# Optimization experiments

Measured on AMD Instinct MI355X. Metric: run time of the kernel, lower is better.

Reference implementation:

```python
import jax, jax.numpy as jnp
import numpy as np

L, N, E, H = 1024, 8, 512, 8  # tgt/src len, batch, embed_dim, num_heads


def setup_inputs() -> dict:
    key = jax.random.key(0)
    ks = jax.random.split(key, 5)
    query = jax.random.normal(ks[0], (L, N, E), dtype=jnp.float32)
    # binary same-agent mask over (tgt, src) positions
    agent_aware_mask = (jax.random.uniform(ks[1], (L, L)) > 0.5).astype(jnp.float32)
    bound = 1.0 / np.sqrt(E)
    # agent-aware dot_product self-attn packs q,k,v,q_same,k_same -> (5E, E)
    in_proj_weight = jax.random.uniform(ks[2], (5 * E, E), jnp.float32, -bound, bound)
    in_proj_bias = jnp.zeros((5 * E,), jnp.float32)
    out_proj_weight = jax.random.uniform(ks[3], (E, E), jnp.float32, -bound, bound)
    out_proj_bias = jnp.zeros((E,), jnp.float32)
    return dict(query=query, in_proj_weight=in_proj_weight, in_proj_bias=in_proj_bias,
                out_proj_weight=out_proj_weight, out_proj_bias=out_proj_bias,
                agent_aware_mask=agent_aware_mask)


def _to_heads(x, tgt_len, bsz, num_heads, head_dim):
    # (L, N, E) -> (N*H, L, head_dim), matching torch's view+transpose
    return x.reshape(tgt_len, bsz * num_heads, head_dim).transpose(1, 0, 2)


def reference(query, in_proj_weight, in_proj_bias, out_proj_weight, out_proj_bias, agent_aware_mask):
    tgt_len, bsz, embed_dim = query.shape
    num_heads = H
    head_dim = embed_dim // num_heads
    scaling = float(head_dim) ** -0.5
    temperature = 1.0

    # packed input projection, chunked into 5: q, k, v, q_same, k_same
    proj = query @ in_proj_weight.T + in_proj_bias
    q, k, v, q_same, k_same = jnp.split(proj, 5, axis=-1)
    q = q * scaling
    q_same = q_same * scaling

    qh = _to_heads(q, tgt_len, bsz, num_heads, head_dim)
    kh = _to_heads(k, tgt_len, bsz, num_heads, head_dim)
    vh = _to_heads(v, tgt_len, bsz, num_heads, head_dim)
    qsh = _to_heads(q_same, tgt_len, bsz, num_heads, head_dim)
    ksh = _to_heads(k_same, tgt_len, bsz, num_heads, head_dim)

    attn_diff = jnp.einsum('bld,bsd->bls', qh, kh)    # cross-agent scores
    attn_same = jnp.einsum('bld,bsd->bls', qsh, ksh)  # same-agent scores

    mask = agent_aware_mask[None, :, :]  # broadcast over (N*H)
    logits = (attn_diff * (1.0 - mask) + attn_same * mask) / temperature

    attn_weights = jax.nn.softmax(logits, axis=-1)
    out = jnp.einsum('bls,bsd->bld', attn_weights, vh)  # (N*H, L, hd)
    out = out.transpose(1, 0, 2).reshape(tgt_len, bsz, embed_dim)
    return out @ out_proj_weight.T + out_proj_bias
```

## Files before the change

kernel.cpp:

```cpp
#include <hip/hip_runtime.h>


typedef float f32x4 __attribute__((ext_vector_type(4)));
typedef short s16x8 __attribute__((ext_vector_type(8)));
typedef unsigned short u16;
typedef u16 u16x4 __attribute__((ext_vector_type(4)));
typedef unsigned int u32x2 __attribute__((ext_vector_type(2)));

#define MFMA16(a, b, c) __builtin_amdgcn_mfma_f32_16x16x32_bf16((a), (b), (c), 0, 0, 0)

__device__ __forceinline__ u16 f2bf(float f) {
  __bf16 h = (__bf16)f;
  return __builtin_bit_cast(u16, h);
}
__device__ __forceinline__ unsigned int pack2(float a, float b) {
  return (unsigned int)f2bf(a) | ((unsigned int)f2bf(b) << 16);
}
__device__ __forceinline__ void gload_lds16(const u16* g, u16* l) {
  __builtin_amdgcn_global_load_lds(
      (const __attribute__((address_space(1))) void*)g,
      (__attribute__((address_space(3))) void*)l, 16, 0, 0);
}

__global__ __launch_bounds__(256) void cvt_swz(const float* __restrict__ in,
                                               u16* __restrict__ out, int n4) {
  int i = blockIdx.x * 256 + threadIdx.x;
  if (i >= n4) return;
  f32x4 v = *(const f32x4*)(in + (size_t)i * 4);
  int e = i << 2;
  int r = e >> 9;
  int k = e & 511;
  int ks = k ^ (((r >> 1) & 3) << 3);
  u16x4 o;
  o[0] = f2bf(v[0]); o[1] = f2bf(v[1]); o[2] = f2bf(v[2]); o[3] = f2bf(v[3]);
  *(u16x4*)(out + ((size_t)r << 9) + ks) = o;
}

__global__ __launch_bounds__(256) void gemm_inproj(
    const u16* __restrict__ X, const u16* __restrict__ W,
    const float* __restrict__ bias,
    u16* __restrict__ Qg, u16* __restrict__ Kg, u16* __restrict__ Vtg,
    u16* __restrict__ Qsg, u16* __restrict__ Ksg) {
  __shared__ __attribute__((aligned(16))) u16 At[128 * 32];
  __shared__ __attribute__((aligned(16))) u16 Bt[128 * 32];
  const int tid = threadIdx.x;
  const int lane = tid & 63, w = tid >> 6;
  const int lr = lane & 15, lq = lane >> 4;
  const int wr = w >> 1, wc = w & 1;
  const int tm = blockIdx.x * 128, tn = blockIdx.y * 128;

  f32x4 acc[4][4] = {};

  for (int k0 = 0; k0 < 512; k0 += 32) {
    if (k0) __syncthreads();
#pragma unroll
    for (int j = 0; j < 2; ++j) {
      const int c = (w * 2 + j) * 64 + lane;
      const int row = c >> 2;
      const int col = (c & 3) * 8;
      gload_lds16(X + (size_t)(tm + row) * 512 + k0 + col, At + (w * 2 + j) * 512);
      gload_lds16(W + (size_t)(tn + row) * 512 + k0 + col, Bt + (w * 2 + j) * 512);
    }
    __syncthreads();
    s16x8 af[4], bf[4];
#pragma unroll
    for (int mi = 0; mi < 4; ++mi) {
      const int row = wr * 64 + mi * 16 + lr;
      const int col = (lq * 8) ^ ((((tm + row) >> 1) & 3) << 3);
      af[mi] = *(const s16x8*)(At + row * 32 + col);
    }
#pragma unroll
    for (int ni = 0; ni < 4; ++ni) {
      const int row = wc * 64 + ni * 16 + lr;
      const int col = (lq * 8) ^ ((((tn + row) >> 1) & 3) << 3);
      bf[ni] = *(const s16x8*)(Bt + row * 32 + col);
    }
#pragma unroll
    for (int mi = 0; mi < 4; ++mi)
#pragma unroll
      for (int ni = 0; ni < 4; ++ni)
        acc[mi][ni] = MFMA16(af[mi], bf[ni], acc[mi][ni]);
  }

  const int chunk = tn >> 9;
  const float qscale = 0.125f * 1.4426950408889634f;
#pragma unroll
  for (int ni = 0; ni < 4; ++ni) {
    const int gc = tn + wc * 64 + ni * 16 + lr;
    const float bv = bias[gc];
    const int e = gc & 511;
    const int hh = e >> 6, dd = e & 63;
#pragma unroll
    for (int mi = 0; mi < 4; ++mi) {
#pragma unroll
      for (int r = 0; r < 4; ++r) {
        const int gr = tm + wr * 64 + mi * 16 + lq * 4 + r;
        const int l = gr >> 3, nn = gr & 7;
        const size_t base = (size_t)(nn * 8 + hh) << 16;
        float v = acc[mi][ni][r] + bv;
        if (chunk == 0) {
          Qg[base + l * 64 + dd] = f2bf(v * qscale);
        } else if (chunk == 3) {
          Qsg[base + l * 64 + dd] = f2bf(v * qscale);
        } else if (chunk == 1) {
          Kg[base + l * 64 + (dd ^ ((l & 7) << 3))] = f2bf(v);
        } else if (chunk == 4) {
          Ksg[base + l * 64 + (dd ^ ((l & 7) << 3))] = f2bf(v);
        } else {
          Vtg[base + (size_t)dd * 1024 + (l ^ ((dd & 7) << 3))] = f2bf(v);
        }
      }
    }
  }
}

__global__ __launch_bounds__(256) void attn_kernel(
    const u16* __restrict__ Qg, const u16* __restrict__ Kg,
    const u16* __restrict__ Vtg, const u16* __restrict__ Qsg,
    const u16* __restrict__ Ksg, const float* __restrict__ mask,
    u16* __restrict__ Og) {
  __shared__ __attribute__((aligned(16))) u16 Kt[64 * 64];
  __shared__ __attribute__((aligned(16))) u16 Kst[64 * 64];
  __shared__ __attribute__((aligned(16))) u16 Vt[64 * 64];
  __shared__ __attribute__((aligned(16))) u16 Pl[4][32 * 72];

  const int tid = threadIdx.x;
  const int lane = tid & 63, w = tid >> 6;
  const int lr = lane & 15, lq = lane >> 4;
  const int bh = blockIdx.y;
  const int q0 = blockIdx.x * 128;
  const size_t bbase = (size_t)bh << 16;
  const int nn = bh >> 3, hh = bh & 7;

  s16x8 qf[2][2], qsf[2][2];
#pragma unroll
  for (int nl = 0; nl < 2; ++nl) {
    const int l = q0 + w * 32 + nl * 16 + lr;
#pragma unroll
    for (int ks = 0; ks < 2; ++ks) {
      qf[nl][ks] = *(const s16x8*)(Qg + bbase + (size_t)l * 64 + ks * 32 + lq * 8);
      qsf[nl][ks] = *(const s16x8*)(Qsg + bbase + (size_t)l * 64 + ks * 32 + lq * 8);
    }
  }

  f32x4 oacc[4][2] = {};
  float m_run[2] = {-1e30f, -1e30f};
  float l_run[2] = {0.f, 0.f};

  for (int t = 0; t < 16; ++t) {
    const int s0 = t * 64;
    if (t) __syncthreads();
#pragma unroll
    for (int j = 0; j < 2; ++j) {
      const int cb = (w * 2 + j) * 64;
      const int c = cb + lane;
      const int row = c >> 3, col = (c & 7) * 8;
      gload_lds16(Kg + bbase + (size_t)(s0 + row) * 64 + col, Kt + cb * 8);
      gload_lds16(Ksg + bbase + (size_t)(s0 + row) * 64 + col, Kst + cb * 8);
      gload_lds16(Vtg + bbase + (size_t)row * 1024 + s0 + col, Vt + cb * 8);
    }
    __syncthreads();

    f32x4 sd[4][2] = {}, ss[4][2] = {};
#pragma unroll
    for (int smi = 0; smi < 4; ++smi) {
      const int srow = smi * 16 + lr;
#pragma unroll
      for (int ks = 0; ks < 2; ++ks) {
        const int off = srow * 64 + ((ks * 32 + lq * 8) ^ ((srow & 7) << 3));
        const s16x8 kf = *(const s16x8*)(Kt + off);
        const s16x8 ksf = *(const s16x8*)(Kst + off);
#pragma unroll
        for (int nl = 0; nl < 2; ++nl) {
          sd[smi][nl] = MFMA16(kf, qf[nl][ks], sd[smi][nl]);
          ss[smi][nl] = MFMA16(ksf, qsf[nl][ks], ss[smi][nl]);
        }
      }
    }

    float mt[2] = {-1e30f, -1e30f};
#pragma unroll
    for (int smi = 0; smi < 4; ++smi) {
#pragma unroll
      for (int nl = 0; nl < 2; ++nl) {
        const int l = q0 + w * 32 + nl * 16 + lr;
        const f32x4 mk =
            *(const f32x4*)(mask + (size_t)l * 1024 + s0 + smi * 16 + lq * 4);
#pragma unroll
        for (int r = 0; r < 4; ++r) {
          const float v = sd[smi][nl][r] + mk[r] * (ss[smi][nl][r] - sd[smi][nl][r]);
          sd[smi][nl][r] = v;
          mt[nl] = fmaxf(mt[nl], v);
        }
      }
    }
#pragma unroll
    for (int nl = 0; nl < 2; ++nl) {
      float m2 = fmaxf(mt[nl], __shfl_xor(mt[nl], 16));
      m2 = fmaxf(m2, __shfl_xor(m2, 32));
      mt[nl] = m2;
    }
    float mnew[2], scale[2];
#pragma unroll
    for (int nl = 0; nl < 2; ++nl) {
      mnew[nl] = fmaxf(m_run[nl], mt[nl]);
      scale[nl] = exp2f(m_run[nl] - mnew[nl]);
      m_run[nl] = mnew[nl];
    }
    float ts[2] = {0.f, 0.f};
#pragma unroll
    for (int smi = 0; smi < 4; ++smi)
#pragma unroll
      for (int nl = 0; nl < 2; ++nl)
#pragma unroll
        for (int r = 0; r < 4; ++r) {
          const float p = exp2f(sd[smi][nl][r] - mnew[nl]);
          sd[smi][nl][r] = p;
          ts[nl] += p;
        }
#pragma unroll
    for (int smi = 0; smi < 4; ++smi)
#pragma unroll
      for (int nl = 0; nl < 2; ++nl) {
        u32x2 pw;
        pw[0] = pack2(sd[smi][nl][0], sd[smi][nl][1]);
        pw[1] = pack2(sd[smi][nl][2], sd[smi][nl][3]);
        *(u32x2*)(&Pl[w][(nl * 16 + lr) * 72 + smi * 16 + lq * 4]) = pw;
      }
#pragma unroll
    for (int nl = 0; nl < 2; ++nl) {
      float s2 = ts[nl] + __shfl_xor(ts[nl], 16);
      s2 += __shfl_xor(s2, 32);
      l_run[nl] = l_run[nl] * scale[nl] + s2;
    }
#pragma unroll
    for (int dmi = 0; dmi < 4; ++dmi)
#pragma unroll
      for (int nl = 0; nl < 2; ++nl) oacc[dmi][nl] = oacc[dmi][nl] * scale[nl];

    asm volatile("s_waitcnt lgkmcnt(0)" ::: "memory");
    __builtin_amdgcn_sched_barrier(0);

#pragma unroll
    for (int ks = 0; ks < 2; ++ks) {
      s16x8 pf[2];
#pragma unroll
      for (int nl = 0; nl < 2; ++nl)
        pf[nl] = *(const s16x8*)(&Pl[w][(nl * 16 + lr) * 72 + ks * 32 + lq * 8]);
#pragma unroll
      for (int dmi = 0; dmi < 4; ++dmi) {
        const int d = dmi * 16 + lr;
        const s16x8 vf =
            *(const s16x8*)(Vt + d * 64 + ((ks * 32 + lq * 8) ^ ((d & 7) << 3)));
#pragma unroll
        for (int nl = 0; nl < 2; ++nl)
          oacc[dmi][nl] = MFMA16(vf, pf[nl], oacc[dmi][nl]);
      }
    }
  }

#pragma unroll
  for (int nl = 0; nl < 2; ++nl) {
    const float inv = 1.0f / l_run[nl];
    const int l = q0 + w * 32 + nl * 16 + lr;
    const int rout = l * 8 + nn;
#pragma unroll
    for (int dmi = 0; dmi < 4; ++dmi)
#pragma unroll
      for (int r = 0; r < 4; ++r) {
        const int d = dmi * 16 + lq * 4 + r;
        const int kout = hh * 64 + d;
        Og[(size_t)rout * 512 + (kout ^ (((rout >> 1) & 3) << 3))] =
            f2bf(oacc[dmi][nl][r] * inv);
      }
  }
}

__global__ __launch_bounds__(256) void gemm_outproj(
    const u16* __restrict__ A, const u16* __restrict__ W,
    const float* __restrict__ bias, float* __restrict__ out) {
  __shared__ __attribute__((aligned(16))) u16 At[128 * 32];
  __shared__ __attribute__((aligned(16))) u16 Bt[128 * 32];
  const int tid = threadIdx.x;
  const int lane = tid & 63, w = tid >> 6;
  const int lr = lane & 15, lq = lane >> 4;
  const int wr = w >> 1, wc = w & 1;
  const int tm = blockIdx.x * 128, tn = blockIdx.y * 128;

  f32x4 acc[4][4] = {};

  for (int k0 = 0; k0 < 512; k0 += 32) {
    if (k0) __syncthreads();
#pragma unroll
    for (int j = 0; j < 2; ++j) {
      const int c = (w * 2 + j) * 64 + lane;
      const int row = c >> 2;
      const int col = (c & 3) * 8;
      gload_lds16(A + (size_t)(tm + row) * 512 + k0 + col, At + (w * 2 + j) * 512);
      gload_lds16(W + (size_t)(tn + row) * 512 + k0 + col, Bt + (w * 2 + j) * 512);
    }
    __syncthreads();
    s16x8 af[4], bf[4];
#pragma unroll
    for (int mi = 0; mi < 4; ++mi) {
      const int row = wr * 64 + mi * 16 + lr;
      const int col = (lq * 8) ^ ((((tm + row) >> 1) & 3) << 3);
      af[mi] = *(const s16x8*)(At + row * 32 + col);
    }
#pragma unroll
    for (int ni = 0; ni < 4; ++ni) {
      const int row = wc * 64 + ni * 16 + lr;
      const int col = (lq * 8) ^ ((((tn + row) >> 1) & 3) << 3);
      bf[ni] = *(const s16x8*)(Bt + row * 32 + col);
    }
#pragma unroll
    for (int mi = 0; mi < 4; ++mi)
#pragma unroll
      for (int ni = 0; ni < 4; ++ni)
        acc[mi][ni] = MFMA16(af[mi], bf[ni], acc[mi][ni]);
  }

#pragma unroll
  for (int ni = 0; ni < 4; ++ni) {
    const int gc = tn + wc * 64 + ni * 16 + lr;
    const float bv = bias[gc];
#pragma unroll
    for (int mi = 0; mi < 4; ++mi)
#pragma unroll
      for (int r = 0; r < 4; ++r) {
        const int gr = tm + wr * 64 + mi * 16 + lq * 4 + r;
        out[(size_t)gr * 512 + gc] = acc[mi][ni][r] + bv;
      }
  }
}

extern "C" void kernel_launch(void* const* d_in, const int* in_sizes, int n_in,
                              void* d_out, int out_size, void* d_ws, size_t ws_size,
                              hipStream_t stream) {
  const float* query = (const float*)d_in[0];
  const float* w_in = (const float*)d_in[1];
  const float* b_in = (const float*)d_in[2];
  const float* w_out = (const float*)d_in[3];
  const float* b_out = (const float*)d_in[4];
  const float* mask = (const float*)d_in[5];

  char* ws = (char*)d_ws;
  u16* Xbf = (u16*)(ws + 0);
  u16* Wbf = (u16*)(ws + 8388608);
  u16* Wobf = (u16*)(ws + 11010048);
  u16* Qg = (u16*)(ws + 11534336);
  u16* Kg = (u16*)(ws + 19922944);
  u16* Vtg = (u16*)(ws + 28311552);
  u16* Qsg = (u16*)(ws + 36700160);
  u16* Ksg = (u16*)(ws + 45088768);
  u16* Og = (u16*)(ws + 53477376);

  hipLaunchKernelGGL(cvt_swz, dim3(4096), dim3(256), 0, stream, query, Xbf, 1048576);
  hipLaunchKernelGGL(cvt_swz, dim3(1280), dim3(256), 0, stream, w_in, Wbf, 327680);
  hipLaunchKernelGGL(cvt_swz, dim3(256), dim3(256), 0, stream, w_out, Wobf, 65536);
  hipLaunchKernelGGL(gemm_inproj, dim3(64, 20), dim3(256), 0, stream,
                     Xbf, Wbf, b_in, Qg, Kg, Vtg, Qsg, Ksg);
  hipLaunchKernelGGL(attn_kernel, dim3(8, 64), dim3(256), 0, stream,
                     Qg, Kg, Vtg, Qsg, Ksg, mask, Og);
  hipLaunchKernelGGL(gemm_outproj, dim3(64, 4), dim3(256), 0, stream,
                     Og, Wobf, b_out, (float*)d_out);
}
```

Before: 218.0 us.

## Bit-pack mask, shrink attention tile, lazy rescale, deeper K-step GEMMs

```diff
diff --git a/kernel.cpp b/kernel.cpp
--- a/kernel.cpp
+++ b/kernel.cpp
@@ -36,13 +36,20 @@
   *(u16x4*)(out + ((size_t)r << 9) + ks) = o;
 }
 
+__global__ __launch_bounds__(256) void mask_pack(const float* __restrict__ m,
+                                                 unsigned long long* __restrict__ out) {
+  int i = blockIdx.x * 256 + threadIdx.x;
+  unsigned long long b = __ballot(m[i] != 0.0f);
+  if ((threadIdx.x & 63) == 0) out[i >> 6] = b;
+}
+
 __global__ __launch_bounds__(256) void gemm_inproj(
     const u16* __restrict__ X, const u16* __restrict__ W,
     const float* __restrict__ bias,
     u16* __restrict__ Qg, u16* __restrict__ Kg, u16* __restrict__ Vtg,
     u16* __restrict__ Qsg, u16* __restrict__ Ksg) {
-  __shared__ __attribute__((aligned(16))) u16 At[128 * 32];
-  __shared__ __attribute__((aligned(16))) u16 Bt[128 * 32];
+  __shared__ __attribute__((aligned(16))) u16 At[128 * 64];
+  __shared__ __attribute__((aligned(16))) u16 Bt[128 * 64];
   const int tid = threadIdx.x;
   const int lane = tid & 63, w = tid >> 6;
   const int lr = lane & 15, lq = lane >> 4;
@@ -51,35 +58,38 @@
 
   f32x4 acc[4][4] = {};
 
-  for (int k0 = 0; k0 < 512; k0 += 32) {
+  for (int k0 = 0; k0 < 512; k0 += 64) {
     if (k0) __syncthreads();
 #pragma unroll
-    for (int j = 0; j < 2; ++j) {
-      const int c = (w * 2 + j) * 64 + lane;
-      const int row = c >> 2;
-      const int col = (c & 3) * 8;
-      gload_lds16(X + (size_t)(tm + row) * 512 + k0 + col, At + (w * 2 + j) * 512);
-      gload_lds16(W + (size_t)(tn + row) * 512 + k0 + col, Bt + (w * 2 + j) * 512);
+    for (int j = 0; j < 4; ++j) {
+      const int c = (w * 4 + j) * 64 + lane;
+      const int row = c >> 3;
+      const int col = (c & 7) * 8;
+      gload_lds16(X + (size_t)(tm + row) * 512 + k0 + col, At + (w * 4 + j) * 512);
+      gload_lds16(W + (size_t)(tn + row) * 512 + k0 + col, Bt + (w * 4 + j) * 512);
     }
     __syncthreads();
-    s16x8 af[4], bf[4];
-#pragma unroll
-    for (int mi = 0; mi < 4; ++mi) {
-      const int row = wr * 64 + mi * 16 + lr;
-      const int col = (lq * 8) ^ ((((tm + row) >> 1) & 3) << 3);
-      af[mi] = *(const s16x8*)(At + row * 32 + col);
-    }
-#pragma unroll
-    for (int ni = 0; ni < 4; ++ni) {
-      const int row = wc * 64 + ni * 16 + lr;
-      const int col = (lq * 8) ^ ((((tn + row) >> 1) & 3) << 3);
-      bf[ni] = *(const s16x8*)(Bt + row * 32 + col);
-    }
-#pragma unroll
-    for (int mi = 0; mi < 4; ++mi)
-#pragma unroll
-      for (int ni = 0; ni < 4; ++ni)
-        acc[mi][ni] = MFMA16(af[mi], bf[ni], acc[mi][ni]);
+#pragma unroll
+    for (int ks = 0; ks < 2; ++ks) {
+      s16x8 af[4], bf[4];
+#pragma unroll
+      for (int mi = 0; mi < 4; ++mi) {
+        const int row = wr * 64 + mi * 16 + lr;
+        const int col = ks * 32 + ((lq * 8) ^ ((((tm + row) >> 1) & 3) << 3));
+        af[mi] = *(const s16x8*)(At + row * 64 + col);
+      }
+#pragma unroll
+      for (int ni = 0; ni < 4; ++ni) {
+        const int row = wc * 64 + ni * 16 + lr;
+        const int col = ks * 32 + ((lq * 8) ^ ((((tn + row) >> 1) & 3) << 3));
+        bf[ni] = *(const s16x8*)(Bt + row * 64 + col);
+      }
+#pragma unroll
+      for (int mi = 0; mi < 4; ++mi)
+#pragma unroll
+        for (int ni = 0; ni < 4; ++ni)
+          acc[mi][ni] = MFMA16(af[mi], bf[ni], acc[mi][ni]);
+    }
   }
 
   const int chunk = tn >> 9;
@@ -114,38 +124,34 @@
   }
 }
 
-__global__ __launch_bounds__(256) void attn_kernel(
+__global__ __launch_bounds__(256, 4) void attn_kernel(
     const u16* __restrict__ Qg, const u16* __restrict__ Kg,
     const u16* __restrict__ Vtg, const u16* __restrict__ Qsg,
-    const u16* __restrict__ Ksg, const float* __restrict__ mask,
+    const u16* __restrict__ Ksg, const unsigned long long* __restrict__ Mp,
     u16* __restrict__ Og) {
   __shared__ __attribute__((aligned(16))) u16 Kt[64 * 64];
   __shared__ __attribute__((aligned(16))) u16 Kst[64 * 64];
   __shared__ __attribute__((aligned(16))) u16 Vt[64 * 64];
-  __shared__ __attribute__((aligned(16))) u16 Pl[4][32 * 72];
+  __shared__ __attribute__((aligned(16))) u16 Pl[4][16 * 72];
 
   const int tid = threadIdx.x;
   const int lane = tid & 63, w = tid >> 6;
   const int lr = lane & 15, lq = lane >> 4;
   const int bh = blockIdx.y;
-  const int q0 = blockIdx.x * 128;
+  const int q0 = blockIdx.x * 64;
   const size_t bbase = (size_t)bh << 16;
   const int nn = bh >> 3, hh = bh & 7;
-
-  s16x8 qf[2][2], qsf[2][2];
-#pragma unroll
-  for (int nl = 0; nl < 2; ++nl) {
-    const int l = q0 + w * 32 + nl * 16 + lr;
-#pragma unroll
-    for (int ks = 0; ks < 2; ++ks) {
-      qf[nl][ks] = *(const s16x8*)(Qg + bbase + (size_t)l * 64 + ks * 32 + lq * 8);
-      qsf[nl][ks] = *(const s16x8*)(Qsg + bbase + (size_t)l * 64 + ks * 32 + lq * 8);
-    }
-  }
-
-  f32x4 oacc[4][2] = {};
-  float m_run[2] = {-1e30f, -1e30f};
-  float l_run[2] = {0.f, 0.f};
+  const int l = q0 + w * 16 + lr;
+
+  s16x8 qf[2], qsf[2];
+#pragma unroll
+  for (int ks = 0; ks < 2; ++ks) {
+    qf[ks] = *(const s16x8*)(Qg + bbase + (size_t)l * 64 + ks * 32 + lq * 8);
+    qsf[ks] = *(const s16x8*)(Qsg + bbase + (size_t)l * 64 + ks * 32 + lq * 8);
+  }
+
+  f32x4 oacc[4] = {};
+  float m_run = -1e30f, l_run = 0.f;
 
   for (int t = 0; t < 16; ++t) {
     const int s0 = t * 64;
@@ -159,170 +165,156 @@
       gload_lds16(Ksg + bbase + (size_t)(s0 + row) * 64 + col, Kst + cb * 8);
       gload_lds16(Vtg + bbase + (size_t)row * 1024 + s0 + col, Vt + cb * 8);
     }
+    const unsigned long long mw = Mp[(size_t)l * 16 + t];
     __syncthreads();
 
-    f32x4 sd[4][2] = {}, ss[4][2] = {};
+    f32x4 sd[4] = {}, ss[4] = {};
+    __builtin_amdgcn_s_setprio(1);
 #pragma unroll
     for (int smi = 0; smi < 4; ++smi) {
       const int srow = smi * 16 + lr;
+      const int sw = (srow & 7) << 3;
 #pragma unroll
       for (int ks = 0; ks < 2; ++ks) {
-        const int off = srow * 64 + ((ks * 32 + lq * 8) ^ ((srow & 7) << 3));
+        const int off = srow * 64 + ((ks * 32 + lq * 8) ^ sw);
         const s16x8 kf = *(const s16x8*)(Kt + off);
-        const s16x8 ksf = *(const s16x8*)(Kst + off);
-#pragma unroll
-        for (int nl = 0; nl < 2; ++nl) {
-          sd[smi][nl] = MFMA16(kf, qf[nl][ks], sd[smi][nl]);
-          ss[smi][nl] = MFMA16(ksf, qsf[nl][ks], ss[smi][nl]);
-        }
-      }
-    }
-
-    float mt[2] = {-1e30f, -1e30f};
+        const s16x8 kfs = *(const s16x8*)(Kst + off);
+        sd[smi] = MFMA16(kf, qf[ks], sd[smi]);
+        ss[smi] = MFMA16(kfs, qsf[ks], ss[smi]);
+      }
+    }
+    __builtin_amdgcn_s_setprio(0);
+
+    float mt = -1e30f;
 #pragma unroll
     for (int smi = 0; smi < 4; ++smi) {
-#pragma unroll
-      for (int nl = 0; nl < 2; ++nl) {
-        const int l = q0 + w * 32 + nl * 16 + lr;
-        const f32x4 mk =
-            *(const f32x4*)(mask + (size_t)l * 1024 + s0 + smi * 16 + lq * 4);
-#pragma unroll
-        for (int r = 0; r < 4; ++r) {
-          const float v = sd[smi][nl][r] + mk[r] * (ss[smi][nl][r] - sd[smi][nl][r]);
-          sd[smi][nl][r] = v;
-          mt[nl] = fmaxf(mt[nl], v);
-        }
-      }
-    }
-#pragma unroll
-    for (int nl = 0; nl < 2; ++nl) {
-      float m2 = fmaxf(mt[nl], __shfl_xor(mt[nl], 16));
-      m2 = fmaxf(m2, __shfl_xor(m2, 32));
-      mt[nl] = m2;
-    }
-    float mnew[2], scale[2];
-#pragma unroll
-    for (int nl = 0; nl < 2; ++nl) {
-      mnew[nl] = fmaxf(m_run[nl], mt[nl]);
-      scale[nl] = exp2f(m_run[nl] - mnew[nl]);
-      m_run[nl] = mnew[nl];
-    }
-    float ts[2] = {0.f, 0.f};
+      const unsigned nib = (unsigned)(mw >> (smi * 16 + lq * 4));
+#pragma unroll
+      for (int r = 0; r < 4; ++r) {
+        const float v = (nib & (1u << r)) ? ss[smi][r] : sd[smi][r];
+        sd[smi][r] = v;
+        mt = fmaxf(mt, v);
+      }
+    }
+    mt = fmaxf(mt, __shfl_xor(mt, 16));
+    mt = fmaxf(mt, __shfl_xor(mt, 32));
+
+    if (!__all(mt <= m_run + 8.0f)) {
+      const float mnew = fmaxf(m_run, mt);
+      const float sc = exp2f(m_run - mnew);
+      m_run = mnew;
+      l_run *= sc;
+#pragma unroll
+      for (int dmi = 0; dmi < 4; ++dmi) oacc[dmi] *= sc;
+    }
+
+    float ts = 0.f;
 #pragma unroll
     for (int smi = 0; smi < 4; ++smi)
 #pragma unroll
-      for (int nl = 0; nl < 2; ++nl)
-#pragma unroll
-        for (int r = 0; r < 4; ++r) {
-          const float p = exp2f(sd[smi][nl][r] - mnew[nl]);
-          sd[smi][nl][r] = p;
-          ts[nl] += p;
-        }
-#pragma unroll
-    for (int smi = 0; smi < 4; ++smi)
-#pragma unroll
-      for (int nl = 0; nl < 2; ++nl) {
-        u32x2 pw;
-        pw[0] = pack2(sd[smi][nl][0], sd[smi][nl][1]);
-        pw[1] = pack2(sd[smi][nl][2], sd[smi][nl][3]);
-        *(u32x2*)(&Pl[w][(nl * 16 + lr) * 72 + smi * 16 + lq * 4]) = pw;
-      }
-#pragma unroll
-    for (int nl = 0; nl < 2; ++nl) {
-      float s2 = ts[nl] + __shfl_xor(ts[nl], 16);
-      s2 += __shfl_xor(s2, 32);
-      l_run[nl] = l_run[nl] * scale[nl] + s2;
-    }
-#pragma unroll
-    for (int dmi = 0; dmi < 4; ++dmi)
-#pragma unroll
-      for (int nl = 0; nl < 2; ++nl) oacc[dmi][nl] = oacc[dmi][nl] * scale[nl];
+      for (int r = 0; r < 4; ++r) {
+        const float p = exp2f(sd[smi][r] - m_run);
+        sd[smi][r] = p;
+        ts += p;
+      }
+#pragma unroll
+    for (int smi = 0; smi < 4; ++smi) {
+      u32x2 pw;
+      pw[0] = pack2(sd[smi][0], sd[smi][1]);
+      pw[1] = pack2(sd[smi][2], sd[smi][3]);
+      *(u32x2*)(&Pl[w][lr * 72 + smi * 16 + lq * 4]) = pw;
+    }
+    ts += __shfl_xor(ts, 16);
+    ts += __shfl_xor(ts, 32);
+    l_run += ts;
 
     asm volatile("s_waitcnt lgkmcnt(0)" ::: "memory");
     __builtin_amdgcn_sched_barrier(0);
 
+    __builtin_amdgcn_s_setprio(1);
 #pragma unroll
     for (int ks = 0; ks < 2; ++ks) {
-      s16x8 pf[2];
-#pragma unroll
-      for (int nl = 0; nl < 2; ++nl)
-        pf[nl] = *(const s16x8*)(&Pl[w][(nl * 16 + lr) * 72 + ks * 32 + lq * 8]);
+      const s16x8 pf = *(const s16x8*)(&Pl[w][lr * 72 + ks * 32 + lq * 8]);
 #pragma unroll
       for (int dmi = 0; dmi < 4; ++dmi) {
         const int d = dmi * 16 + lr;
         const s16x8 vf =
             *(const s16x8*)(Vt + d * 64 + ((ks * 32 + lq * 8) ^ ((d & 7) << 3)));
-#pragma unroll
-        for (int nl = 0; nl < 2; ++nl)
-          oacc[dmi][nl] = MFMA16(vf, pf[nl], oacc[dmi][nl]);
-      }
-    }
-  }
-
-#pragma unroll
-  for (int nl = 0; nl < 2; ++nl) {
-    const float inv = 1.0f / l_run[nl];
-    const int l = q0 + w * 32 + nl * 16 + lr;
-    const int rout = l * 8 + nn;
-#pragma unroll
-    for (int dmi = 0; dmi < 4; ++dmi)
-#pragma unroll
-      for (int r = 0; r < 4; ++r) {
-        const int d = dmi * 16 + lq * 4 + r;
-        const int kout = hh * 64 + d;
-        Og[(size_t)rout * 512 + (kout ^ (((rout >> 1) & 3) << 3))] =
-            f2bf(oacc[dmi][nl][r] * inv);
-      }
+        oacc[dmi] = MFMA16(vf, pf, oacc[dmi]);
+      }
+    }
+    __builtin_amdgcn_s_setprio(0);
+  }
+
+  const float inv = 1.0f / l_run;
+  const int rout = l * 8 + nn;
+  const int swzr = ((rout >> 1) & 3) << 3;
+#pragma unroll
+  for (int dmi = 0; dmi < 4; ++dmi) {
+    u16x4 o;
+#pragma unroll
+    for (int r = 0; r < 4; ++r) o[r] = f2bf(oacc[dmi][r] * inv);
+    const int kout = (hh * 64 + dmi * 16 + lq * 4) ^ swzr;
+    *(u16x4*)(Og + (size_t)rout * 512 + kout) = o;
   }
 }
 
 __global__ __launch_bounds__(256) void gemm_outproj(
     const u16* __restrict__ A, const u16* __restrict__ W,
     const float* __restrict__ bias, float* __restrict__ out) {
-  __shared__ __attribute__((aligned(16))) u16 At[128 * 32];
-  __shared__ __attribute__((aligned(16))) u16 Bt[128 * 32];
+  __shared__ __attribute__((aligned(16))) u16 At[128 * 64];
+  __shared__ __attribute__((aligned(16))) u16 Bt[64 * 64];
   const int tid = threadIdx.x;
   const int lane = tid & 63, w = tid >> 6;
   const int lr = lane & 15, lq = lane >> 4;
   const int wr = w >> 1, wc = w & 1;
-  const int tm = blockIdx.x * 128, tn = blockIdx.y * 128;
-
-  f32x4 acc[4][4] = {};
-
-  for (int k0 = 0; k0 < 512; k0 += 32) {
+  const int tm = blockIdx.x * 128, tn = blockIdx.y * 64;
+
+  f32x4 acc[4][2] = {};
+
+  for (int k0 = 0; k0 < 512; k0 += 64) {
     if (k0) __syncthreads();
+#pragma unroll
+    for (int j = 0; j < 4; ++j) {
+      const int c = (w * 4 + j) * 64 + lane;
+      const int row = c >> 3;
+      const int col = (c & 7) * 8;
+      gload_lds16(A + (size_t)(tm + row) * 512 + k0 + col, At + (w * 4 + j) * 512);
+    }
 #pragma unroll
     for (int j = 0; j < 2; ++j) {
       const int c = (w * 2 + j) * 64 + lane;
-      const int row = c >> 2;
-      const int col = (c & 3) * 8;
-      gload_lds16(A + (size_t)(tm + row) * 512 + k0 + col, At + (w * 2 + j) * 512);
+      const int row = c >> 3;
+      const int col = (c & 7) * 8;
       gload_lds16(W + (size_t)(tn + row) * 512 + k0 + col, Bt + (w * 2 + j) * 512);
     }
     __syncthreads();
-    s16x8 af[4], bf[4];
-#pragma unroll
-    for (int mi = 0; mi < 4; ++mi) {
-      const int row = wr * 64 + mi * 16 + lr;
-      const int col = (lq * 8) ^ ((((tm + row) >> 1) & 3) << 3);
-      af[mi] = *(const s16x8*)(At + row * 32 + col);
-    }
-#pragma unroll
-    for (int ni = 0; ni < 4; ++ni) {
-      const int row = wc * 64 + ni * 16 + lr;
-      const int col = (lq * 8) ^ ((((tn + row) >> 1) & 3) << 3);
-      bf[ni] = *(const s16x8*)(Bt + row * 32 + col);
-    }
-#pragma unroll
-    for (int mi = 0; mi < 4; ++mi)
-#pragma unroll
-      for (int ni = 0; ni < 4; ++ni)
-        acc[mi][ni] = MFMA16(af[mi], bf[ni], acc[mi][ni]);
-  }
-
-#pragma unroll
-  for (int ni = 0; ni < 4; ++ni) {
-    const int gc = tn + wc * 64 + ni * 16 + lr;
+#pragma unroll
+    for (int ks = 0; ks < 2; ++ks) {
+      s16x8 af[4], bf[2];
+#pragma unroll
+      for (int mi = 0; mi < 4; ++mi) {
+        const int row = wr * 64 + mi * 16 + lr;
+        const int col = ks * 32 + ((lq * 8) ^ ((((tm + row) >> 1) & 3) << 3));
+        af[mi] = *(const s16x8*)(At + row * 64 + col);
+      }
+#pragma unroll
+      for (int ni = 0; ni < 2; ++ni) {
+        const int row = wc * 32 + ni * 16 + lr;
+        const int col = ks * 32 + ((lq * 8) ^ ((((tn + row) >> 1) & 3) << 3));
+        bf[ni] = *(const s16x8*)(Bt + row * 64 + col);
+      }
+#pragma unroll
+      for (int mi = 0; mi < 4; ++mi)
+#pragma unroll
+        for (int ni = 0; ni < 2; ++ni)
+          acc[mi][ni] = MFMA16(af[mi], bf[ni], acc[mi][ni]);
+    }
+  }
+
+#pragma unroll
+  for (int ni = 0; ni < 2; ++ni) {
+    const int gc = tn + wc * 32 + ni * 16 + lr;
     const float bv = bias[gc];
 #pragma unroll
     for (int mi = 0; mi < 4; ++mi)
@@ -354,14 +346,16 @@
   u16* Qsg = (u16*)(ws + 36700160);
   u16* Ksg = (u16*)(ws + 45088768);
   u16* Og = (u16*)(ws + 53477376);
+  unsigned long long* Mp = (unsigned long long*)(ws + 0);
 
   hipLaunchKernelGGL(cvt_swz, dim3(4096), dim3(256), 0, stream, query, Xbf, 1048576);
   hipLaunchKernelGGL(cvt_swz, dim3(1280), dim3(256), 0, stream, w_in, Wbf, 327680);
   hipLaunchKernelGGL(cvt_swz, dim3(256), dim3(256), 0, stream, w_out, Wobf, 65536);
   hipLaunchKernelGGL(gemm_inproj, dim3(64, 20), dim3(256), 0, stream,
                      Xbf, Wbf, b_in, Qg, Kg, Vtg, Qsg, Ksg);
-  hipLaunchKernelGGL(attn_kernel, dim3(8, 64), dim3(256), 0, stream,
-                     Qg, Kg, Vtg, Qsg, Ksg, mask, Og);
-  hipLaunchKernelGGL(gemm_outproj, dim3(64, 4), dim3(256), 0, stream,
+  hipLaunchKernelGGL(mask_pack, dim3(4096), dim3(256), 0, stream, mask, Mp);
+  hipLaunchKernelGGL(attn_kernel, dim3(16, 64), dim3(256), 0, stream,
+                     Qg, Kg, Vtg, Qsg, Ksg, Mp, Og);
+  hipLaunchKernelGGL(gemm_outproj, dim3(64, 8), dim3(256), 0, stream,
                      Og, Wobf, b_out, (float*)d_out);
 }
```

After: 200.7 us. 8.0% less time.
